# Kernel tuning notes

Measured on AMD Instinct MI355X. Metric: run time of the kernel, lower is better.

Reference implementation:

```python
import jax, jax.numpy as jnp
import numpy as np

N_HEAD = 16
NEG_BIG = 1e10  # matches the module's -10000000000.0 masking constant


def setup_inputs() -> dict:
    key = jax.random.key(0)
    k1, k2, k3 = jax.random.split(key, 3)
    B, S, D = 2, 2048, 1024
    std = 0.02
    return {
        "x": jax.random.normal(k1, (B, S, D), dtype=jnp.float32),
        "c_attn_w": jax.random.normal(k2, (D, 3 * D), dtype=jnp.float32) * std,
        "c_attn_b": jnp.zeros((3 * D,), dtype=jnp.float32),
        "c_proj_w": jax.random.normal(k3, (D, D), dtype=jnp.float32) * std,
        "c_proj_b": jnp.zeros((D,), dtype=jnp.float32),
    }


def reference(x, c_attn_w, c_attn_b, c_proj_w, c_proj_b):
    B, S, D = x.shape
    H = N_HEAD
    Dh = D // H

    # c_attn: fused QKV projection (Conv1D == linear)
    qkv = jnp.einsum("bsd,df->bsf", x, c_attn_w) + c_attn_b  # [B,S,3D]
    q, k, v = jnp.split(qkv, 3, axis=-1)

    def split_heads(t):  # [B,S,D] -> [B,H,S,Dh]
        return t.reshape(B, S, H, Dh).transpose(0, 2, 1, 3)

    q, k, v = split_heads(q), split_heads(k), split_heads(v)
    present = jnp.stack([k, v], axis=1)  # [B,2,H,S,Dh]

    # scores: explicit O(S^2) matrix, scaled by sqrt(head_dim)
    w = jnp.einsum("bhqd,bhkd->bhqk", q, k) / jnp.sqrt(
        jnp.asarray(Dh, dtype=q.dtype)
    )  # [B,H,S,S]

    # causal mask, applied exactly as in the source: w*mask - 1e10*(1-mask)
    mask = jnp.tril(jnp.ones((S, S), dtype=w.dtype))[None, None]  # [1,1,S,S]
    w = w * mask - NEG_BIG * (1.0 - mask)

    w = jax.nn.softmax(w, axis=-1)
    a = jnp.einsum("bhqk,bhkd->bhqd", w, v)  # [B,H,S,Dh]

    # merge heads: [B,H,S,Dh] -> [B,S,D]
    a = a.transpose(0, 2, 1, 3).reshape(B, S, D)

    # output projection
    a = jnp.einsum("bsd,df->bsf", a, c_proj_w) + c_proj_b
    return (a, present)
```

## Files before the change

kernel.cpp:

```cpp
#include <hip/hip_runtime.h>
#include <hip/hip_bf16.h>
#include <stdint.h>

typedef __bf16 bf16_t;
typedef __bf16 bf16x8 __attribute__((ext_vector_type(8)));
typedef __bf16 bf16x4v __attribute__((ext_vector_type(4)));
typedef float f32x4 __attribute__((ext_vector_type(4)));

#define MFMA16(A, B, C) __builtin_amdgcn_mfma_f32_16x16x32_bf16((A), (B), (C), 0, 0, 0)

#define BB 2
#define SS 2048
#define DD 1024
#define HH 16
#define DH 64
#define MM (BB * SS)

__device__ __forceinline__ void load_lds16(const void* g, void* l) {
  __builtin_amdgcn_global_load_lds(
      (const __attribute__((address_space(1))) void*)g,
      (__attribute__((address_space(3))) void*)l, 16, 0, 0);
}

__device__ __forceinline__ float fast_exp2(float x) {
  float r;
  asm("v_exp_f32 %0, %1" : "=v"(r) : "v"(x));
  return r;
}
__device__ __forceinline__ uint32_t cvt_pk_bf16(float lo, float hi) {
  uint32_t u;
  asm("v_cvt_pk_bf16_f32 %0, %1, %2" : "=v"(u) : "v"(lo), "v"(hi));
  return u;
}


__global__ __launch_bounds__(256) void cvt_f32_to_bf16(const float* __restrict__ in,
                                                       bf16_t* __restrict__ out, int n4) {
  int i = blockIdx.x * blockDim.x + threadIdx.x;
  if (i >= n4) return;
  float4 v = reinterpret_cast<const float4*>(in)[i];
  bf16x4v o;
  o[0] = (bf16_t)v.x; o[1] = (bf16_t)v.y; o[2] = (bf16_t)v.z; o[3] = (bf16_t)v.w;
  reinterpret_cast<bf16x4v*>(out)[i] = o;
}

__global__ void transpose_f32_to_bf16(const float* __restrict__ W, bf16_t* __restrict__ WT,
                                      int K, int N) {
  __shared__ float tile[32][33];
  int n0 = blockIdx.x * 32, k0 = blockIdx.y * 32;
  int tx = threadIdx.x, ty = threadIdx.y;
  #pragma unroll
  for (int i = ty; i < 32; i += 8) tile[i][tx] = W[(size_t)(k0 + i) * N + n0 + tx];
  __syncthreads();
  #pragma unroll
  for (int i = ty; i < 32; i += 8) WT[(size_t)(n0 + i) * K + k0 + tx] = (bf16_t)tile[tx][i];
}

template <int BM, int BN, int WGM, int WGN, int EPI>
__global__ __launch_bounds__(512) void gemm2(
    const bf16_t* __restrict__ A, const bf16_t* __restrict__ BT,
    const float* __restrict__ bias, float* __restrict__ outf,
    bf16_t* __restrict__ q_b, bf16_t* __restrict__ k_b, bf16_t* __restrict__ vt_b,
    int M, int N, int K) {
  constexpr int BK = 64;
  constexpr int MF = BM / WGM / 16;
  constexpr int NF = BN / WGN / 16;
  constexpr int RS = BM / WGM;
  constexpr int CS = BN / WGN;
  constexpr int LA = BM * BK * 2 / (512 * 16);
  constexpr int LB = BN * BK * 2 / (512 * 16);

  __shared__ __align__(16) bf16_t At[2][BM * BK];
  __shared__ __align__(16) bf16_t Bt[2][BN * BK];

  const int tid = threadIdx.x;
  const int l = tid & 63, w = tid >> 6;
  const int lr = l & 15, lg = l >> 4;
  const int wr = w / WGN, wc = w % WGN;
  const int row0 = blockIdx.y * BM, col0 = blockIdx.x * BN;

  auto stage = [&](int buf, int k0) {
    #pragma unroll
    for (int i = 0; i < LA; ++i) {
      int e = (tid + i * 512) * 8;
      int r = e >> 6, c = e & 63;
      int cs = ((c * 2) ^ ((r & 7) << 4)) >> 1;
      load_lds16(&A[(size_t)(row0 + r) * K + k0 + cs], &At[buf][(w * 64 + i * 512) * 8]);
    }
    #pragma unroll
    for (int i = 0; i < LB; ++i) {
      int e = (tid + i * 512) * 8;
      int r = e >> 6, c = e & 63;
      int cs = ((c * 2) ^ ((r & 7) << 4)) >> 1;
      load_lds16(&BT[(size_t)(col0 + r) * K + k0 + cs], &Bt[buf][(w * 64 + i * 512) * 8]);
    }
  };

  f32x4 vz = {0.f, 0.f, 0.f, 0.f};
  f32x4 acc[MF][NF];
  #pragma unroll
  for (int m = 0; m < MF; ++m)
    #pragma unroll
    for (int n = 0; n < NF; ++n) acc[m][n] = vz;

  const int sw = (lr & 7) << 4;
  const int nk = K / BK;
  stage(0, 0);
  __syncthreads();
  int cur = 0;
  for (int k = 0; k < nk; ++k) {
    if (k + 1 < nk) stage(cur ^ 1, (k + 1) * BK);
    #pragma unroll
    for (int kk = 0; kk < 2; ++kk) {
      const int rdo = (kk * 64 + lg * 16) ^ sw;
      bf16x8 af[MF], bfr[NF];
      #pragma unroll
      for (int m = 0; m < MF; ++m) {
        int row = wr * RS + m * 16 + lr;
        af[m] = *(const bf16x8*)((const char*)&At[cur][0] + row * 128 + rdo);
      }
      #pragma unroll
      for (int n = 0; n < NF; ++n) {
        int brow = wc * CS + n * 16 + lr;
        bfr[n] = *(const bf16x8*)((const char*)&Bt[cur][0] + brow * 128 + rdo);
      }
      #pragma unroll
      for (int m = 0; m < MF; ++m)
        #pragma unroll
        for (int n = 0; n < NF; ++n) acc[m][n] = MFMA16(af[m], bfr[n], acc[m][n]);
    }
    __syncthreads();
    cur ^= 1;
  }

  #pragma unroll
  for (int m = 0; m < MF; ++m) {
    int rl = wr * RS + m * 16 + lg * 4;
    #pragma unroll
    for (int n = 0; n < NF; ++n) {
      int col = col0 + wc * CS + n * 16 + lr;
      float bz = bias[col];
      #pragma unroll
      for (int r = 0; r < 4; ++r) {
        int row = row0 + rl + r;
        float v = acc[m][n][r] + bz;
        if (EPI == 1) {
          outf[(size_t)row * N + col] = v;
        } else {
          int b = row >> 11, s = row & 2047;
          int part = col >> 10, d = col & 1023;
          int h = d >> 6, dh = d & 63;
          size_t idx = ((size_t)(b * HH + h) * SS + s) * DH + dh;
          if (part == 0) {
            q_b[idx] = (bf16_t)v;
          } else if (part == 1) {
            k_b[idx] = (bf16_t)v;
            outf[(((size_t)(b * 2 + 0) * HH + h) * SS + s) * DH + dh] = v;
          } else {
            vt_b[((size_t)(b * HH + h) * DH + dh) * SS + s] = (bf16_t)v;
            outf[(((size_t)(b * 2 + 1) * HH + h) * SS + s) * DH + dh] = v;
          }
        }
      }
    }
  }
}

__global__ __launch_bounds__(256) void attn_fwd(
    const bf16_t* __restrict__ q_b, const bf16_t* __restrict__ k_b,
    const bf16_t* __restrict__ vt_b, bf16_t* __restrict__ attn_out) {
  __shared__ __align__(16) bf16_t Kt[2][64 * 64];
  __shared__ __align__(16) bf16_t Vt[2][64 * 64];
  __shared__ __align__(16) bf16_t P_lds[4][32][72];

  const int bh = blockIdx.y;
  const int q0b = (gridDim.x - 1 - blockIdx.x) * 128;
  const int tid = threadIdx.x;
  const int w = tid >> 6, l = tid & 63;
  const int lr = l & 15, lg = l >> 4;

  const bf16_t* qb = q_b + (size_t)bh * SS * DH;
  const bf16_t* kb = k_b + (size_t)bh * SS * DH;
  const bf16_t* vt = vt_b + (size_t)bh * DH * SS;

  const int r0 = tid >> 3;
  const int cs = (((tid & 7) * 16) ^ ((r0 & 7) << 4)) >> 1;
  const bf16_t* gk0 = kb + r0 * DH + cs;
  const bf16_t* gk1 = gk0 + 32 * DH;
  const bf16_t* gv0 = vt + (size_t)r0 * SS + cs;
  const bf16_t* gv1 = gv0 + 32 * SS;
  auto stageKV = [&](int buf) {
    bf16_t* lk = &Kt[buf][w * 512];
    load_lds16(gk0, lk);
    load_lds16(gk1, lk + 2048);
    bf16_t* lv = &Vt[buf][w * 512];
    load_lds16(gv0, lv);
    load_lds16(gv1, lv + 2048);
    gk0 += 64 * DH; gk1 += 64 * DH; gv0 += 64; gv1 += 64;
  };

  const int qrow0 = q0b + w * 32 + lr;
  const int qrow1 = qrow0 + 16;
  bf16x8 qf[2][2];
  qf[0][0] = *(const bf16x8*)&qb[(size_t)qrow0 * DH + lg * 8];
  qf[0][1] = *(const bf16x8*)&qb[(size_t)qrow0 * DH + 32 + lg * 8];
  qf[1][0] = *(const bf16x8*)&qb[(size_t)qrow1 * DH + lg * 8];
  qf[1][1] = *(const bf16x8*)&qb[(size_t)qrow1 * DH + 32 + lg * 8];

  bf16x8 ones;
  #pragma unroll
  for (int j = 0; j < 8; ++j) ones[j] = (bf16_t)1.0f;

  f32x4 vzero = {0.f, 0.f, 0.f, 0.f};
  f32x4 oacc[2][4];
  #pragma unroll
  for (int q = 0; q < 2; ++q)
    #pragma unroll
    for (int d = 0; d < 4; ++d) oacc[q][d] = vzero;
  float m_run[2] = {-1e30f, -1e30f}, l_run[2] = {0.f, 0.f};

  const float SCL = 0.125f * 1.4426950408889634f;
  const int sw = (lr & 7) << 4;
  const int rd0 = (lg * 16) ^ sw;
  const int rd1 = (64 + lg * 16) ^ sw;

  const int nkv = q0b / 64 + 2;
  stageKV(0);
  __syncthreads();
  int cur = 0;
  for (int t = 0; t < nkv; ++t) {
    const int kv0 = t * 64;
    if (t + 1 < nkv) stageKV(cur ^ 1);

    float sc[2][4][4];
    #pragma unroll
    for (int kvf = 0; kvf < 4; ++kvf) {
      const char* kbase = (const char*)&Kt[cur][0] + (kvf * 16 + lr) * 128;
      bf16x8 kf0 = *(const bf16x8*)(kbase + rd0);
      bf16x8 kf1 = *(const bf16x8*)(kbase + rd1);
      #pragma unroll
      for (int q = 0; q < 2; ++q) {
        f32x4 a = vzero;
        a = MFMA16(kf0, qf[q][0], a);
        a = MFMA16(kf1, qf[q][1], a);
        #pragma unroll
        for (int r = 0; r < 4; ++r) sc[q][kvf][r] = a[r];
      }
    }
    if (kv0 + 63 > q0b + w * 32) {
      #pragma unroll
      for (int q = 0; q < 2; ++q) {
        int dthr = (q ? qrow1 : qrow0) - kv0;
        #pragma unroll
        for (int kvf = 0; kvf < 4; ++kvf)
          #pragma unroll
          for (int r = 0; r < 4; ++r) {
            int kvl = kvf * 16 + lg * 4 + r;
            if (kvl > dthr) sc[q][kvf][r] = -1e30f;
          }
      }
    }

    #pragma unroll
    for (int q = 0; q < 2; ++q) {
      float tm = fmaxf(fmaxf(sc[q][0][0], sc[q][0][1]), sc[q][0][2]);
      tm = fmaxf(fmaxf(tm, sc[q][0][3]), sc[q][1][0]);
      tm = fmaxf(fmaxf(tm, sc[q][1][1]), sc[q][1][2]);
      tm = fmaxf(fmaxf(tm, sc[q][1][3]), sc[q][2][0]);
      tm = fmaxf(fmaxf(tm, sc[q][2][1]), sc[q][2][2]);
      tm = fmaxf(fmaxf(tm, sc[q][2][3]), sc[q][3][0]);
      tm = fmaxf(fmaxf(tm, sc[q][3][1]), sc[q][3][2]);
      tm = fmaxf(tm, sc[q][3][3]);
      tm = fmaxf(tm, __shfl_xor(tm, 16));
      tm = fmaxf(tm, __shfl_xor(tm, 32));
      if (!__all(tm <= m_run[q] + 44.0f)) {
        float mnew = fmaxf(m_run[q], tm);
        float alpha = fast_exp2((m_run[q] - mnew) * SCL);
        l_run[q] *= alpha;
        #pragma unroll
        for (int d = 0; d < 4; ++d) oacc[q][d] *= alpha;
        m_run[q] = mnew;
      }
      float mneg = m_run[q] * (-SCL);
      #pragma unroll
      for (int kvf = 0; kvf < 4; ++kvf) {
        float p0 = fast_exp2(__builtin_fmaf(sc[q][kvf][0], SCL, mneg));
        float p1 = fast_exp2(__builtin_fmaf(sc[q][kvf][1], SCL, mneg));
        float p2 = fast_exp2(__builtin_fmaf(sc[q][kvf][2], SCL, mneg));
        float p3 = fast_exp2(__builtin_fmaf(sc[q][kvf][3], SCL, mneg));
        uint2 pk;
        pk.x = cvt_pk_bf16(p0, p1);
        pk.y = cvt_pk_bf16(p2, p3);
        *(uint2*)&P_lds[w][q * 16 + lr][kvf * 16 + lg * 4] = pk;
      }
    }

    bf16x8 pf[2][2];
    #pragma unroll
    for (int q = 0; q < 2; ++q) {
      pf[q][0] = *(const bf16x8*)&P_lds[w][q * 16 + lr][lg * 8];
      pf[q][1] = *(const bf16x8*)&P_lds[w][q * 16 + lr][32 + lg * 8];
      f32x4 ls = vzero;
      ls = MFMA16(ones, pf[q][0], ls);
      ls = MFMA16(ones, pf[q][1], ls);
      l_run[q] += ls[0];
    }
    __builtin_amdgcn_s_setprio(1);
    #pragma unroll
    for (int d = 0; d < 4; ++d) {
      const char* vbase = (const char*)&Vt[cur][0] + (d * 16 + lr) * 128;
      bf16x8 vf0 = *(const bf16x8*)(vbase + rd0);
      bf16x8 vf1 = *(const bf16x8*)(vbase + rd1);
      #pragma unroll
      for (int q = 0; q < 2; ++q) {
        oacc[q][d] = MFMA16(vf0, pf[q][0], oacc[q][d]);
        oacc[q][d] = MFMA16(vf1, pf[q][1], oacc[q][d]);
      }
    }
    __builtin_amdgcn_s_setprio(0);
    __syncthreads();
    cur ^= 1;
  }

  const int b = bh >> 4, h = bh & 15;
  #pragma unroll
  for (int q = 0; q < 2; ++q) {
    float inv_l = 1.f / l_run[q];
    int qrow = q ? qrow1 : qrow0;
    #pragma unroll
    for (int d = 0; d < 4; ++d)
      #pragma unroll
      for (int r = 0; r < 4; ++r) {
        int dd = d * 16 + lg * 4 + r;
        attn_out[((size_t)(b * SS + qrow)) * DD + h * DH + dd] =
            (bf16_t)(oacc[q][d][r] * inv_l);
      }
  }
}

extern "C" void kernel_launch(void* const* d_in, const int* in_sizes, int n_in,
                              void* d_out, int out_size, void* d_ws, size_t ws_size,
                              hipStream_t stream) {
  const float* x = (const float*)d_in[0];
  const float* c_attn_w = (const float*)d_in[1];
  const float* c_attn_b = (const float*)d_in[2];
  const float* c_proj_w = (const float*)d_in[3];
  const float* c_proj_b = (const float*)d_in[4];

  float* out = (float*)d_out;
  float* present = out + (size_t)BB * SS * DD;

  char* ws = (char*)d_ws;
  bf16_t* xb     = (bf16_t*)(ws + 0);
  bf16_t* wqkvT  = (bf16_t*)(ws + 8388608);
  bf16_t* wprojT = (bf16_t*)(ws + 14680064);
  bf16_t* q_b    = (bf16_t*)(ws + 16777216);
  bf16_t* k_b    = (bf16_t*)(ws + 25165824);
  bf16_t* vt_b   = (bf16_t*)(ws + 33554432);
  bf16_t* attn_o = (bf16_t*)(ws + 41943040);

  cvt_f32_to_bf16<<<(MM * DD / 4 + 255) / 256, 256, 0, stream>>>(x, xb, MM * DD / 4);
  transpose_f32_to_bf16<<<dim3(3 * DD / 32, DD / 32), dim3(32, 8), 0, stream>>>(
      c_attn_w, wqkvT, DD, 3 * DD);
  transpose_f32_to_bf16<<<dim3(DD / 32, DD / 32), dim3(32, 8), 0, stream>>>(
      c_proj_w, wprojT, DD, DD);
  gemm2<256, 192, 4, 2, 0><<<dim3(3 * DD / 192, MM / 256), 512, 0, stream>>>(
      xb, wqkvT, c_attn_b, present, q_b, k_b, vt_b, MM, 3 * DD, DD);
  attn_fwd<<<dim3(SS / 128, BB * HH), 256, 0, stream>>>(q_b, k_b, vt_b, attn_o);
  gemm2<128, 128, 2, 4, 1><<<dim3(DD / 128, MM / 128), 512, 0, stream>>>(
      attn_o, wprojT, c_proj_b, out, nullptr, nullptr, nullptr, MM, DD, DD);
}
```

Before: 225.2 us.

## Pair long and short causal query tiles per attention block for load balance

Each attention block now handles two 64-row query tiles, one near the end of the sequence (j mirrored) and one near the start, instead of one contiguous 128-row tile. Every block therefore walks a similar total of KV tiles, which evens out causal work across blocks. The short tile's MFMA and softmax work is skipped once its causal range ends. The cost is a runtime-variable q loop and per-warp branches, which may add register pressure and divergence. Each block also does fewer useful MFMAs per KV stage on later iterations.

```diff
diff --git a/kernel.cpp b/kernel.cpp
--- a/kernel.cpp
+++ b/kernel.cpp
@@ -174,7 +174,9 @@
   __shared__ __align__(16) bf16_t P_lds[4][32][72];
 
   const int bh = blockIdx.y;
-  const int q0b = (gridDim.x - 1 - blockIdx.x) * 128;
+  const int j = blockIdx.x;
+  const int qlb = (31 - j) * 64;
+  const int qsb = j * 64;
   const int tid = threadIdx.x;
   const int w = tid >> 6, l = tid & 63;
   const int lr = l & 15, lg = l >> 4;
@@ -199,8 +201,8 @@
     gk0 += 64 * DH; gk1 += 64 * DH; gv0 += 64; gv1 += 64;
   };
 
-  const int qrow0 = q0b + w * 32 + lr;
-  const int qrow1 = qrow0 + 16;
+  const int qrow0 = qlb + w * 16 + lr;
+  const int qrow1 = qsb + w * 16 + lr;
   bf16x8 qf[2][2];
   qf[0][0] = *(const bf16x8*)&qb[(size_t)qrow0 * DH + lg * 8];
   qf[0][1] = *(const bf16x8*)&qb[(size_t)qrow0 * DH + 32 + lg * 8];
@@ -209,7 +211,7 @@
 
   bf16x8 ones;
   #pragma unroll
-  for (int j = 0; j < 8; ++j) ones[j] = (bf16_t)1.0f;
+  for (int jj = 0; jj < 8; ++jj) ones[jj] = (bf16_t)1.0f;
 
   f32x4 vzero = {0.f, 0.f, 0.f, 0.f};
   f32x4 oacc[2][4];
@@ -224,13 +226,14 @@
   const int rd0 = (lg * 16) ^ sw;
   const int rd1 = (64 + lg * 16) ^ sw;
 
-  const int nkv = q0b / 64 + 2;
+  const int nkv = 32 - j;
   stageKV(0);
   __syncthreads();
   int cur = 0;
   for (int t = 0; t < nkv; ++t) {
     const int kv0 = t * 64;
     if (t + 1 < nkv) stageKV(cur ^ 1);
+    const bool act1 = (t <= j);
 
     float sc[2][4][4];
     #pragma unroll
@@ -238,31 +241,44 @@
       const char* kbase = (const char*)&Kt[cur][0] + (kvf * 16 + lr) * 128;
       bf16x8 kf0 = *(const bf16x8*)(kbase + rd0);
       bf16x8 kf1 = *(const bf16x8*)(kbase + rd1);
-      #pragma unroll
-      for (int q = 0; q < 2; ++q) {
+      {
         f32x4 a = vzero;
-        a = MFMA16(kf0, qf[q][0], a);
-        a = MFMA16(kf1, qf[q][1], a);
-        #pragma unroll
-        for (int r = 0; r < 4; ++r) sc[q][kvf][r] = a[r];
-      }
-    }
-    if (kv0 + 63 > q0b + w * 32) {
-      #pragma unroll
-      for (int q = 0; q < 2; ++q) {
-        int dthr = (q ? qrow1 : qrow0) - kv0;
-        #pragma unroll
-        for (int kvf = 0; kvf < 4; ++kvf)
-          #pragma unroll
-          for (int r = 0; r < 4; ++r) {
-            int kvl = kvf * 16 + lg * 4 + r;
-            if (kvl > dthr) sc[q][kvf][r] = -1e30f;
-          }
-      }
-    }
-
-    #pragma unroll
-    for (int q = 0; q < 2; ++q) {
+        a = MFMA16(kf0, qf[0][0], a);
+        a = MFMA16(kf1, qf[0][1], a);
+        #pragma unroll
+        for (int r = 0; r < 4; ++r) sc[0][kvf][r] = a[r];
+      }
+      if (act1) {
+        f32x4 a = vzero;
+        a = MFMA16(kf0, qf[1][0], a);
+        a = MFMA16(kf1, qf[1][1], a);
+        #pragma unroll
+        for (int r = 0; r < 4; ++r) sc[1][kvf][r] = a[r];
+      }
+    }
+    if (kv0 + 63 > qlb + w * 16) {
+      int dthr = qrow0 - kv0;
+      #pragma unroll
+      for (int kvf = 0; kvf < 4; ++kvf)
+        #pragma unroll
+        for (int r = 0; r < 4; ++r) {
+          int kvl = kvf * 16 + lg * 4 + r;
+          if (kvl > dthr) sc[0][kvf][r] = -1e30f;
+        }
+    }
+    if (act1 && kv0 + 63 > qsb + w * 16) {
+      int dthr = qrow1 - kv0;
+      #pragma unroll
+      for (int kvf = 0; kvf < 4; ++kvf)
+        #pragma unroll
+        for (int r = 0; r < 4; ++r) {
+          int kvl = kvf * 16 + lg * 4 + r;
+          if (kvl > dthr) sc[1][kvf][r] = -1e30f;
+        }
+    }
+
+    const int nq = act1 ? 2 : 1;
+    for (int q = 0; q < nq; ++q) {
       float tm = fmaxf(fmaxf(sc[q][0][0], sc[q][0][1]), sc[q][0][2]);
       tm = fmaxf(fmaxf(tm, sc[q][0][3]), sc[q][1][0]);
       tm = fmaxf(fmaxf(tm, sc[q][1][1]), sc[q][1][2]);
@@ -296,8 +312,7 @@
     }
 
     bf16x8 pf[2][2];
-    #pragma unroll
-    for (int q = 0; q < 2; ++q) {
+    for (int q = 0; q < nq; ++q) {
       pf[q][0] = *(const bf16x8*)&P_lds[w][q * 16 + lr][lg * 8];
       pf[q][1] = *(const bf16x8*)&P_lds[w][q * 16 + lr][32 + lg * 8];
       f32x4 ls = vzero;
@@ -311,10 +326,11 @@
       const char* vbase = (const char*)&Vt[cur][0] + (d * 16 + lr) * 128;
       bf16x8 vf0 = *(const bf16x8*)(vbase + rd0);
       bf16x8 vf1 = *(const bf16x8*)(vbase + rd1);
-      #pragma unroll
-      for (int q = 0; q < 2; ++q) {
-        oacc[q][d] = MFMA16(vf0, pf[q][0], oacc[q][d]);
-        oacc[q][d] = MFMA16(vf1, pf[q][1], oacc[q][d]);
+      oacc[0][d] = MFMA16(vf0, pf[0][0], oacc[0][d]);
+      oacc[0][d] = MFMA16(vf1, pf[0][1], oacc[0][d]);
+      if (act1) {
+        oacc[1][d] = MFMA16(vf0, pf[1][0], oacc[1][d]);
+        oacc[1][d] = MFMA16(vf1, pf[1][1], oacc[1][d]);
       }
     }
     __builtin_amdgcn_s_setprio(0);
@@ -366,7 +382,7 @@
       c_proj_w, wprojT, DD, DD);
   gemm2<256, 192, 4, 2, 0><<<dim3(3 * DD / 192, MM / 256), 512, 0, stream>>>(
       xb, wqkvT, c_attn_b, present, q_b, k_b, vt_b, MM, 3 * DD, DD);
-  attn_fwd<<<dim3(SS / 128, BB * HH), 256, 0, stream>>>(q_b, k_b, vt_b, attn_o);
+  attn_fwd<<<dim3(16, BB * HH), 256, 0, stream>>>(q_b, k_b, vt_b, attn_o);
   gemm2<128, 128, 2, 4, 1><<<dim3(DD / 128, MM / 128), 512, 0, stream>>>(
       attn_o, wprojT, c_proj_b, out, nullptr, nullptr, nullptr, MM, DD, DD);
 }
```

Measured after the change: 538.6 us. 2.39x slower.
